# Kernel tuning notes

Hardware: AMD Instinct MI355X
Metric: run time of the kernel (lower is better)

Reference implementation:

```python
import jax, jax.numpy as jnp
import numpy as np

N = 100_000      # nodes
E = 1_600_000    # edges (avg degree 16)
H = 128          # hidden_dim
L = 2            # num_layers
G = 64           # graphs in batch
BN_EPS = 1e-5


def setup_inputs() -> dict:
    key = jax.random.key(0)
    ks = jax.random.split(key, 20)
    x = jax.random.normal(ks[0], (N, 1), jnp.float32)
    edge_index = jax.random.randint(ks[1], (2, E), 0, N, dtype=jnp.int64)
    edge_attr = jax.random.uniform(ks[2], (E, 1), jnp.float32)
    batch = jnp.sort(jax.random.randint(ks[3], (N,), 0, G, dtype=jnp.int64))
    s = 1.0 / np.sqrt(H)
    return {
        "x": x, "edge_index": edge_index, "edge_attr": edge_attr, "batch": batch,
        "enc_w": jax.random.normal(ks[4], (1, H), jnp.float32),
        "enc_b": jnp.zeros((H,), jnp.float32),
        "eenc_w": jax.random.normal(ks[5], (1, H), jnp.float32),
        "eenc_b": jnp.zeros((H,), jnp.float32),
        "eps": jnp.zeros((L,), jnp.float32),  # train_eps=True, init 0
        "w1": jax.random.normal(ks[6], (L, H, H), jnp.float32) * s,
        "b1": jnp.zeros((L, H), jnp.float32),
        "w2": jax.random.normal(ks[7], (L, H, H), jnp.float32) * s,
        "b2": jnp.zeros((L, H), jnp.float32),
        "gamma": jnp.ones((L, H), jnp.float32),
        "beta": jnp.zeros((L, H), jnp.float32),
        "cw1": jax.random.normal(ks[8], (H, H // 2), jnp.float32) * s,
        "cb1": jnp.zeros((H // 2,), jnp.float32),
        "cw2": jax.random.normal(ks[9], (H // 2, 1), jnp.float32) * (1.0 / np.sqrt(H // 2)),
        "cb2": jnp.zeros((1,), jnp.float32),
    }


def reference(x, edge_index, edge_attr, batch,
              enc_w, enc_b, eenc_w, eenc_b,
              eps, w1, b1, w2, b2, gamma, beta,
              cw1, cb1, cw2, cb2):
    # Inference mode: dropout = identity, BatchNorm uses running stats (mean=0, var=1).
    h = x @ enc_w + enc_b                 # [N, H] node encoder
    ea = edge_attr @ eenc_w + eenc_b      # [E, H] edge encoder
    src, dst = edge_index[0], edge_index[1]
    inv_std = 1.0 / jnp.sqrt(1.0 + BN_EPS)
    for l in range(L):
        # GINEConv: out = MLP((1+eps)*x + sum_j relu(x_j + e_ij))
        msg = jax.nn.relu(h[src] + ea)                         # [E, H] gather + fuse
        agg = jax.ops.segment_sum(msg, dst, num_segments=N)    # [N, H] scatter-sum
        z = (1.0 + eps[l]) * h + agg
        z = jax.nn.relu(z @ w1[l] + b1[l]) @ w2[l] + b2[l]      # GIN MLP
        h = jax.nn.relu(gamma[l] * z * inv_std + beta[l])       # BN (eval) + ReLU
    # global mean pool over graphs
    cnt = jax.ops.segment_sum(jnp.ones((N, 1), h.dtype), batch, num_segments=G)
    pooled = jax.ops.segment_sum(h, batch, num_segments=G) / jnp.maximum(cnt, 1.0)
    hc = jax.nn.relu(pooled @ cw1 + cb1)
    out = jax.nn.sigmoid(hc @ cw2 + cb2)
    return out.squeeze(-1)                # [G]
```

## Files before the change

### kernel.cpp

```cpp
#include <hip/hip_runtime.h>

#define HDIM 128
#define NGRAPH 64
#define INVSTD 0.99999500003749972f
#define WTPAD 136
#define WSLOT (128 * WTPAD)
#define BKN 512
#define EPB 4096

typedef unsigned short ushort_t;
typedef unsigned int uint_t;
typedef unsigned char uchar_t;
typedef __attribute__((ext_vector_type(8))) short bf16x8;
typedef __attribute__((ext_vector_type(4))) float f32x4;
typedef __attribute__((ext_vector_type(2))) float f32x2;

__device__ __forceinline__ float bf2f(uint_t u) {
    return __int_as_float((int)(u << 16));
}
__device__ __forceinline__ float bf2f_hi(uint_t u) {
    return __int_as_float((int)(u & 0xFFFF0000u));
}
__device__ __forceinline__ uint_t f2bf(float f) {
    uint_t x = __float_as_uint(f);
    return (x + 0x7FFFu + ((x >> 16) & 1u)) >> 16;
}
__device__ __forceinline__ uint_t pack2(float a, float b) {
    return f2bf(a) | (f2bf(b) << 16);
}
__device__ __forceinline__ uint_t pack4fp8(float a, float b, float c, float d) {
    int v = __builtin_amdgcn_cvt_pk_fp8_f32(a, b, 0, false);
    v = __builtin_amdgcn_cvt_pk_fp8_f32(c, d, v, true);
    return (uint_t)v;
}

__global__ void k_encode(const float* __restrict__ x, const float* __restrict__ ew,
                         const float* __restrict__ enb, const float* __restrict__ ebe,
                         ushort_t* __restrict__ hb, uchar_t* __restrict__ hq, int N) {
    int tid = blockIdx.x * blockDim.x + threadIdx.x;
    int stride = gridDim.x * blockDim.x;
    int q = tid & 15;
    float4 wa = ((const float4*)ew)[2 * q];
    float4 wb = ((const float4*)ew)[2 * q + 1];
    float4 ba = ((const float4*)enb)[2 * q];
    float4 bb = ((const float4*)enb)[2 * q + 1];
    float4 ea = ((const float4*)ebe)[2 * q];
    float4 eb2 = ((const float4*)ebe)[2 * q + 1];
    ba.x += ea.x; ba.y += ea.y; ba.z += ea.z; ba.w += ea.w;
    bb.x += eb2.x; bb.y += eb2.y; bb.z += eb2.z; bb.w += eb2.w;
    int total = N * 16;
    for (int t = tid; t < total; t += stride) {
        int n = t >> 4;
        float xv = x[n];
        float v0 = fmaf(xv, wa.x, ba.x), v1 = fmaf(xv, wa.y, ba.y);
        float v2 = fmaf(xv, wa.z, ba.z), v3 = fmaf(xv, wa.w, ba.w);
        float v4 = fmaf(xv, wb.x, bb.x), v5 = fmaf(xv, wb.y, bb.y);
        float v6 = fmaf(xv, wb.z, bb.z), v7 = fmaf(xv, wb.w, bb.w);
        uint4 o;
        o.x = pack2(v0, v1); o.y = pack2(v2, v3);
        o.z = pack2(v4, v5); o.w = pack2(v6, v7);
        ((uint4*)(hb + (size_t)n * HDIM))[q] = o;
        uint2 o8;
        o8.x = pack4fp8(v0, v1, v2, v3);
        o8.y = pack4fp8(v4, v5, v6, v7);
        ((uint2*)(hq + (size_t)n * HDIM))[q] = o8;
    }
}

__global__ void k_prepw(const float* __restrict__ w1, const float* __restrict__ w2,
                        ushort_t* __restrict__ wtg) {
    int t = blockIdx.x * 256 + threadIdx.x;
    if (t >= 4 * 16384) return;
    int w = t >> 14, idx = t & 16383;
    int k = idx >> 7, n = idx & 127;
    const float* src = ((w & 1) ? w2 : w1) + (size_t)(w >> 1) * 16384;
    wtg[(size_t)w * WSLOT + n * WTPAD + k] = (ushort_t)f2bf(src[idx]);
}

__global__ __launch_bounds__(256) void k_cnt(const int* __restrict__ ei, int* __restrict__ btot,
                                             int nb, int E) {
    __shared__ int hist[256];
    hist[threadIdx.x] = 0;
    __syncthreads();
    int e0 = blockIdx.x * EPB;
    for (int i = threadIdx.x; i < EPB; i += 256) {
        int e = e0 + i;
        if (e < E) atomicAdd(&hist[ei[E + e] / BKN], 1);
    }
    __syncthreads();
    int c = hist[threadIdx.x];
    if (threadIdx.x < nb && c > 0) atomicAdd(&btot[threadIdx.x], c);
}

__global__ void k_bscan(const int* __restrict__ btot, int* __restrict__ segs, int nb, int E) {
    __shared__ int sm[256];
    int t = threadIdx.x;
    int v = (t < nb) ? btot[t] : 0;
    sm[t] = v;
    __syncthreads();
    #pragma unroll
    for (int off = 1; off < 256; off <<= 1) {
        int u = (t >= off) ? sm[t - off] : 0;
        __syncthreads();
        sm[t] += u;
        __syncthreads();
    }
    if (t < nb) segs[t] = sm[t] - v;
    if (t == 0) segs[nb] = E;
}

__global__ __launch_bounds__(256) void k_place0(const int* __restrict__ ei,
                                                const float* __restrict__ attr,
                                                const int* __restrict__ segs, int* cursor,
                                                int4* __restrict__ ebuf, int nb, int E) {
    __shared__ int hist[256];
    __shared__ int basev[256];
    hist[threadIdx.x] = 0;
    __syncthreads();
    int e0 = blockIdx.x * EPB;
    for (int i = threadIdx.x; i < EPB; i += 256) {
        int e = e0 + i;
        if (e < E) atomicAdd(&hist[ei[E + e] / BKN], 1);
    }
    __syncthreads();
    {
        int c = hist[threadIdx.x];
        basev[threadIdx.x] = (threadIdx.x < nb && c > 0) ? atomicAdd(&cursor[threadIdx.x], c) : 0;
        hist[threadIdx.x] = 0;
    }
    __syncthreads();
    for (int i = threadIdx.x; i < EPB; i += 256) {
        int e = e0 + i;
        if (e < E) {
            int s = ei[e], d = ei[E + e];
            float a = attr[e];
            int b = d / BKN;
            int r = atomicAdd(&hist[b], 1);
            ebuf[segs[b] + basev[b] + r] = make_int4(s, __float_as_int(a), d, 0);
        }
    }
}

__global__ __launch_bounds__(256) void k_fine(const int4* __restrict__ ebuf,
                                              const int* __restrict__ segs,
                                              int2* __restrict__ epack, int* __restrict__ rs,
                                              int nb, int N, int E) {
    __shared__ int hist[BKN];
    __shared__ int cur[BKN];
    __shared__ int psum[256];
    int b = blockIdx.x;
    int d0 = b * BKN;
    int nd = min(BKN, N - d0);
    for (int i = threadIdx.x; i < BKN; i += 256) hist[i] = 0;
    __syncthreads();
    int s0 = segs[b], s1 = segs[b + 1];
    for (int e = s0 + threadIdx.x; e < s1; e += 256)
        atomicAdd(&hist[ebuf[e].z - d0], 1);
    __syncthreads();
    int h0 = hist[2 * threadIdx.x], h1 = hist[2 * threadIdx.x + 1];
    psum[threadIdx.x] = h0 + h1;
    __syncthreads();
    #pragma unroll
    for (int off = 1; off < 256; off <<= 1) {
        int u = (threadIdx.x >= off) ? psum[threadIdx.x - off] : 0;
        __syncthreads();
        psum[threadIdx.x] += u;
        __syncthreads();
    }
    int pb = psum[threadIdx.x] - (h0 + h1);
    cur[2 * threadIdx.x] = pb;
    cur[2 * threadIdx.x + 1] = pb + h0;
    __syncthreads();
    for (int i = threadIdx.x; i < nd; i += 256) rs[d0 + i] = s0 + cur[i];
    if (b == nb - 1 && threadIdx.x == 0) rs[N] = E;
    __syncthreads();
    for (int e = s0 + threadIdx.x; e < s1; e += 256) {
        int4 rec = ebuf[e];
        int r = atomicAdd(&cur[rec.z - d0], 1);
        epack[s0 + r] = make_int2(rec.x, rec.y);
    }
}

__device__ __forceinline__ void acc_edge(float acc[8], const uint2& u, float at,
        const float4& wa, const float4& wb) {
    f32x2 p0 = __builtin_amdgcn_cvt_pk_f32_fp8(u.x, false);
    f32x2 p1 = __builtin_amdgcn_cvt_pk_f32_fp8(u.x, true);
    f32x2 p2 = __builtin_amdgcn_cvt_pk_f32_fp8(u.y, false);
    f32x2 p3 = __builtin_amdgcn_cvt_pk_f32_fp8(u.y, true);
    acc[0] += fmaxf(fmaf(at, wa.x, p0[0]), 0.f);
    acc[1] += fmaxf(fmaf(at, wa.y, p0[1]), 0.f);
    acc[2] += fmaxf(fmaf(at, wa.z, p1[0]), 0.f);
    acc[3] += fmaxf(fmaf(at, wa.w, p1[1]), 0.f);
    acc[4] += fmaxf(fmaf(at, wb.x, p2[0]), 0.f);
    acc[5] += fmaxf(fmaf(at, wb.y, p2[1]), 0.f);
    acc[6] += fmaxf(fmaf(at, wb.z, p3[0]), 0.f);
    acc[7] += fmaxf(fmaf(at, wb.w, p3[1]), 0.f);
}

__global__ __launch_bounds__(256) void k_agg(
    const uchar_t* __restrict__ hq, const ushort_t* __restrict__ hb,
    const int* __restrict__ rs, const int2* __restrict__ epack,
    const float* __restrict__ ew, const float* __restrict__ ebv,
    const float* __restrict__ epsp, ushort_t* __restrict__ zb, int N) {
    int wave = (blockIdx.x * 256 + threadIdx.x) >> 6;
    if (wave >= N) return;
    int lane = threadIdx.x & 63;
    int p = lane >> 4;
    int q = lane & 15;
    int n = wave;
    int beg = rs[n];
    int cntE = rs[n + 1] - beg;
    float4 wa = ((const float4*)ew)[2 * q], wb = ((const float4*)ew)[2 * q + 1];

    float acc[8] = {0.f, 0.f, 0.f, 0.f, 0.f, 0.f, 0.f, 0.f};
    float acc2[8] = {0.f, 0.f, 0.f, 0.f, 0.f, 0.f, 0.f, 0.f};
    int j = p;
    for (; j + 4 < cntE; j += 8) {
        int2 e1 = epack[beg + j];
        int2 e2 = epack[beg + j + 4];
        uint2 u1 = *(const uint2*)(hq + (size_t)e1.x * HDIM + q * 8);
        uint2 u2 = *(const uint2*)(hq + (size_t)e2.x * HDIM + q * 8);
        acc_edge(acc,  u1, __int_as_float(e1.y), wa, wb);
        acc_edge(acc2, u2, __int_as_float(e2.y), wa, wb);
    }
    if (j < cntE) {
        int2 e1 = epack[beg + j];
        uint2 u1 = *(const uint2*)(hq + (size_t)e1.x * HDIM + q * 8);
        acc_edge(acc, u1, __int_as_float(e1.y), wa, wb);
    }
    #pragma unroll
    for (int k = 0; k < 8; ++k) {
        float v = acc[k] + acc2[k];
        v += __shfl_xor(v, 16);
        v += __shfl_xor(v, 32);
        acc[k] = v;
    }
    if (p == 0) {
        float sc = 1.f + epsp[0];
        float4 ba = ((const float4*)ebv)[2 * q], bb = ((const float4*)ebv)[2 * q + 1];
        float s0 = sc * ba.x, s1 = sc * ba.y, s2 = sc * ba.z, s3 = sc * ba.w;
        float s4 = sc * bb.x, s5 = sc * bb.y, s6 = sc * bb.z, s7 = sc * bb.w;
        uint4 u = *(const uint4*)(hb + (size_t)n * HDIM + q * 8);
        uint4 ob;
        ob.x = pack2(fmaf(sc, bf2f(u.x & 0xFFFFu), acc[0]) - s0,
                     fmaf(sc, bf2f_hi(u.x),        acc[1]) - s1);
        ob.y = pack2(fmaf(sc, bf2f(u.y & 0xFFFFu), acc[2]) - s2,
                     fmaf(sc, bf2f_hi(u.y),        acc[3]) - s3);
        ob.z = pack2(fmaf(sc, bf2f(u.z & 0xFFFFu), acc[4]) - s4,
                     fmaf(sc, bf2f_hi(u.z),        acc[5]) - s5);
        ob.w = pack2(fmaf(sc, bf2f(u.w & 0xFFFFu), acc[6]) - s6,
                     fmaf(sc, bf2f_hi(u.w),        acc[7]) - s7);
        *(uint4*)(zb + (size_t)n * HDIM + q * 8) = ob;
    }
}

template<int MODE, int EBF, int WQ>
__global__ __launch_bounds__(256) void k_gemm(
    const ushort_t* __restrict__ A, const ushort_t* __restrict__ WT,
    const float* __restrict__ bias, const float* __restrict__ gam,
    const float* __restrict__ bet, const float* __restrict__ ebe,
    ushort_t* __restrict__ out, uchar_t* __restrict__ outq, int N) {
    __shared__ ushort_t wt[128 * WTPAD];
    int tid = threadIdx.x;
    #pragma unroll
    for (int i = 0; i < 9; ++i) {
        int c = i * 256 + tid;
        if (c < 2176) ((bf16x8*)wt)[c] = ((const bf16x8*)WT)[c];
    }
    __syncthreads();

    int wid = tid >> 6, lane = tid & 63;
    int ra = lane & 15, qa = lane >> 4;

    bf16x8 bfr[4][8];
    #pragma unroll
    for (int ks = 0; ks < 4; ++ks)
        #pragma unroll
        for (int nf = 0; nf < 8; ++nf)
            bfr[ks][nf] = *(const bf16x8*)&wt[(nf * 16 + ra) * WTPAD + ks * 32 + qa * 8];

    float bi[8], gg[8], be_[8], ef[8];
    #pragma unroll
    for (int nf = 0; nf < 8; ++nf) {
        int col = nf * 16 + ra;
        bi[nf] = bias[col];
        if (MODE == 1) { gg[nf] = gam[col]; be_[nf] = bet[col]; }
        if (EBF)       { ef[nf] = ebe[col]; }
    }

    bf16x8 azero;
    #pragma unroll
    for (int j = 0; j < 8; ++j) azero[j] = 0;

    #pragma unroll
    for (int it = 0; it < 4; ++it) {
        int m0 = blockIdx.x * 256 + it * 64 + wid * 16;
        int mr = m0 + ra;
        bf16x8 afr[4];
        #pragma unroll
        for (int ks = 0; ks < 4; ++ks)
            afr[ks] = (mr < N) ? *(const bf16x8*)&A[(size_t)mr * HDIM + ks * 32 + qa * 8]
                               : azero;
        f32x4 acc[8];
        #pragma unroll
        for (int nf = 0; nf < 8; ++nf)
            #pragma unroll
            for (int j = 0; j < 4; ++j) acc[nf][j] = 0.f;
        #pragma unroll
        for (int ks = 0; ks < 4; ++ks)
            #pragma unroll
            for (int nf = 0; nf < 8; ++nf)
                acc[nf] = __builtin_amdgcn_mfma_f32_16x16x32_bf16(afr[ks], bfr[ks][nf], acc[nf], 0, 0, 0);
        #pragma unroll
        for (int nf = 0; nf < 8; ++nf) {
            #pragma unroll
            for (int r = 0; r < 4; ++r) {
                int row = m0 + qa * 4 + r;
                if (row < N) {
                    float v = acc[nf][r] + bi[nf];
                    if (MODE == 0) v = fmaxf(v, 0.f);
                    else           v = fmaxf(fmaf(gg[nf] * v, INVSTD, be_[nf]), 0.f);
                    if (EBF)       v += ef[nf];
                    out[(size_t)row * HDIM + nf * 16 + ra] = (ushort_t)f2bf(v);
                    if (WQ)
                        outq[(size_t)row * HDIM + nf * 16 + ra] =
                            (uchar_t)(__builtin_amdgcn_cvt_pk_fp8_f32(v, 0.f, 0, false) & 0xFF);
                }
            }
        }
    }
}

#define PCHUNK 256
#define PWIN 4
__global__ __launch_bounds__(256) void k_pool2(const ushort_t* __restrict__ hb,
                                               const int* __restrict__ batch,
                                               float* pooled, int N) {
    __shared__ float acc[PWIN][HDIM];
    int n0 = blockIdx.x * PCHUNK;
    if (n0 >= N) return;
    int n1 = min(n0 + PCHUNK, N);
    int g0 = batch[n0];
    int g1 = batch[n1 - 1];
    for (int i = threadIdx.x; i < PWIN * HDIM; i += 256) ((float*)acc)[i] = 0.f;
    __syncthreads();

    int grp = threadIdx.x >> 5;
    int q = threadIdx.x & 31;
    float4 racc = make_float4(0.f, 0.f, 0.f, 0.f);
    int gcur = g0;
    for (int n = n0 + grp; n < n1; n += 8) {
        int g = batch[n];
        if (g != gcur) {
            int w = gcur - g0;
            float* p = (w < PWIN) ? &acc[w][q * 4] : (pooled + gcur * HDIM + q * 4);
            atomicAdd(p + 0, racc.x); atomicAdd(p + 1, racc.y);
            atomicAdd(p + 2, racc.z); atomicAdd(p + 3, racc.w);
            racc = make_float4(0.f, 0.f, 0.f, 0.f);
            gcur = g;
        }
        uint2 u = ((const uint2*)(hb + (size_t)n * HDIM))[q];
        racc.x += bf2f(u.x);
        racc.y += bf2f_hi(u.x);
        racc.z += bf2f(u.y);
        racc.w += bf2f_hi(u.y);
    }
    {
        int w = gcur - g0;
        float* p = (w < PWIN) ? &acc[w][q * 4] : (pooled + gcur * HDIM + q * 4);
        atomicAdd(p + 0, racc.x); atomicAdd(p + 1, racc.y);
        atomicAdd(p + 2, racc.z); atomicAdd(p + 3, racc.w);
    }
    __syncthreads();

    int span = min(g1 - g0 + 1, PWIN);
    for (int i = threadIdx.x; i < span * HDIM; i += 256) {
        int w = i >> 7, f = i & 127;
        float v = acc[w][f];
        if (v != 0.f) atomicAdd(pooled + (g0 + w) * HDIM + f, v);
    }
}

__global__ void k_classify(const float* __restrict__ pooled, const int* __restrict__ batch,
                           const float* __restrict__ cw1, const float* __restrict__ cb1,
                           const float* __restrict__ cw2, const float* __restrict__ cb2,
                           float* __restrict__ out, int N) {
    __shared__ float p[HDIM];
    int g = blockIdx.x, j = threadIdx.x;
    int lo = 0, hi = N;
    while (lo < hi) { int m = (lo + hi) >> 1; if (batch[m] < g) lo = m + 1; else hi = m; }
    int lo2 = lo, hi2 = N;
    while (lo2 < hi2) { int m = (lo2 + hi2) >> 1; if (batch[m] < g + 1) lo2 = m + 1; else hi2 = m; }
    float c = fmaxf((float)(lo2 - lo), 1.f);
    p[j]      = pooled[g * HDIM + j] / c;
    p[j + 64] = pooled[g * HDIM + j + 64] / c;
    __syncthreads();
    float acc = cb1[j];
    #pragma unroll 4
    for (int k = 0; k < HDIM; ++k) acc = fmaf(p[k], cw1[k * 64 + j], acc);
    acc = fmaxf(acc, 0.f);
    float v = acc * cw2[j];
    #pragma unroll
    for (int off = 32; off > 0; off >>= 1) v += __shfl_down(v, off, 64);
    if (j == 0) out[g] = 1.f / (1.f + expf(-(v + cb2[0])));
}

static inline size_t align_up(size_t v, size_t a) { return (v + a - 1) & ~(a - 1); }

extern "C" void kernel_launch(void* const* d_in, const int* in_sizes, int n_in,
                              void* d_out, int out_size, void* d_ws, size_t ws_size,
                              hipStream_t stream) {
    const float* x      = (const float*)d_in[0];
    const int*   ei     = (const int*)d_in[1];
    const float* eattr  = (const float*)d_in[2];
    const int*   batch  = (const int*)d_in[3];
    const float* enc_w  = (const float*)d_in[4];
    const float* enc_b  = (const float*)d_in[5];
    const float* eenc_w = (const float*)d_in[6];
    const float* eenc_b = (const float*)d_in[7];
    const float* eps    = (const float*)d_in[8];
    const float* w1     = (const float*)d_in[9];
    const float* b1     = (const float*)d_in[10];
    const float* w2     = (const float*)d_in[11];
    const float* b2     = (const float*)d_in[12];
    const float* gamma  = (const float*)d_in[13];
    const float* beta   = (const float*)d_in[14];
    const float* cw1    = (const float*)d_in[15];
    const float* cb1    = (const float*)d_in[16];
    const float* cw2    = (const float*)d_in[17];
    const float* cb2    = (const float*)d_in[18];

    int N = in_sizes[0];
    int E = in_sizes[2];

    int nb = (N + BKN - 1) / BKN;
    int nblk = (E + EPB - 1) / EPB;

    char* wsb = (char*)d_ws;
    size_t off = 0;
    ushort_t* hb  = (ushort_t*)(wsb + off); off = align_up(off + (size_t)N * HDIM * 2, 256);
    uchar_t*  hq  = (uchar_t*)(wsb + off);  off = align_up(off + (size_t)N * HDIM, 256);
    ushort_t* zb  = (ushort_t*)(wsb + off); off = align_up(off + (size_t)N * HDIM * 2, 256);
    ushort_t* wtg = (ushort_t*)(wsb + off); off = align_up(off + (size_t)4 * WSLOT * 2, 256);
    float* pooled = (float*)(wsb + off);    off = align_up(off + NGRAPH * HDIM * 4, 256);
    int*   btot   = (int*)(wsb + off);      off = align_up(off + (size_t)(nb + 1) * 4, 256);
    int*   segs   = (int*)(wsb + off);      off = align_up(off + (size_t)(nb + 1) * 4, 256);
    int*   cursor = (int*)(wsb + off);      off = align_up(off + (size_t)nb * 4, 256);
    int*   rs     = (int*)(wsb + off);      off = align_up(off + (size_t)(N + 1) * 4, 256);
    int4*  ebuf   = (int4*)(wsb + off);     off = align_up(off + (size_t)E * 16, 256);
    int2*  epack  = (int2*)(wsb + off);     off = align_up(off + (size_t)E * 8, 256);

    hipMemsetAsync(btot, 0, (size_t)(nb + 1) * 4, stream);
    hipMemsetAsync(cursor, 0, (size_t)nb * 4, stream);
    k_cnt<<<nblk, 256, 0, stream>>>(ei, btot, nb, E);
    k_prepw<<<256, 256, 0, stream>>>(w1, w2, wtg);
    k_bscan<<<1, 256, 0, stream>>>(btot, segs, nb, E);
    k_place0<<<nblk, 256, 0, stream>>>(ei, eattr, segs, cursor, ebuf, nb, E);
    k_fine<<<nb, 256, 0, stream>>>(ebuf, segs, epack, rs, nb, N, E);

    hipMemsetAsync(pooled, 0, NGRAPH * HDIM * sizeof(float), stream);
    k_encode<<<2048, 256, 0, stream>>>(x, enc_w, enc_b, eenc_b, hb, hq, N);

    int gblocks = (N + 255) / 256;
    int ablocks = (N * 64 + 255) / 256;

    k_agg<<<ablocks, 256, 0, stream>>>(hq, hb, rs, epack, eenc_w, eenc_b, eps + 0, zb, N);
    k_gemm<0,0,0><<<gblocks, 256, 0, stream>>>(zb, wtg + 0 * WSLOT, b1, nullptr, nullptr,
                                               nullptr, zb, nullptr, N);
    k_gemm<1,1,1><<<gblocks, 256, 0, stream>>>(zb, wtg + 1 * WSLOT, b2, gamma, beta,
                                               eenc_b, hb, hq, N);
    k_agg<<<ablocks, 256, 0, stream>>>(hq, hb, rs, epack, eenc_w, eenc_b, eps + 1, zb, N);
    k_gemm<0,0,0><<<gblocks, 256, 0, stream>>>(zb, wtg + 2 * WSLOT, b1 + HDIM, nullptr, nullptr,
                                               nullptr, zb, nullptr, N);
    k_gemm<1,0,0><<<gblocks, 256, 0, stream>>>(zb, wtg + 3 * WSLOT, b2 + HDIM, gamma + HDIM,
                                               beta + HDIM, nullptr, hb, nullptr, N);

    k_pool2<<<(N + PCHUNK - 1) / PCHUNK, 256, 0, stream>>>(hb, batch, pooled, N);
    k_classify<<<NGRAPH, 64, 0, stream>>>(pooled, batch, cw1, cb1, cw2, cb2, (float*)d_out, N);
}
```

Before: 302.9 us.

## Fuse the two GIN MLP GEMMs into one kernel with intermediate in LDS

Merges the two per-layer GEMM launches into a single k_mlp kernel. Each wave computes its 16-row tile of the first linear+ReLU and writes it to its own slice of shared memory, then runs the second GEMM with the BN, ReLU and output epilogue from there. This removes a global round trip of the intermediate activation and one launch per layer. In exchange, weight fragments are now read directly from global memory per wave instead of being staged in LDS, and each block covers fewer rows.

```diff
diff --git a/kernel.cpp b/kernel.cpp
--- a/kernel.cpp
+++ b/kernel.cpp
@@ -254,47 +254,32 @@
     }
 }
 
-template<int MODE, int EBF, int WQ>
-__global__ __launch_bounds__(256) void k_gemm(
-    const ushort_t* __restrict__ A, const ushort_t* __restrict__ WT,
-    const float* __restrict__ bias, const float* __restrict__ gam,
-    const float* __restrict__ bet, const float* __restrict__ ebe,
+template<int EBF, int WQ>
+__global__ __launch_bounds__(512) void k_mlp(
+    const ushort_t* __restrict__ A, const ushort_t* __restrict__ WT1,
+    const ushort_t* __restrict__ WT2,
+    const float* __restrict__ b1v, const float* __restrict__ b2v,
+    const float* __restrict__ gam, const float* __restrict__ bet,
+    const float* __restrict__ ebe,
     ushort_t* __restrict__ out, uchar_t* __restrict__ outq, int N) {
-    __shared__ ushort_t wt[128 * WTPAD];
+    __shared__ ushort_t tls[128 * WTPAD];
     int tid = threadIdx.x;
-    #pragma unroll
-    for (int i = 0; i < 9; ++i) {
-        int c = i * 256 + tid;
-        if (c < 2176) ((bf16x8*)wt)[c] = ((const bf16x8*)WT)[c];
-    }
-    __syncthreads();
-
     int wid = tid >> 6, lane = tid & 63;
     int ra = lane & 15, qa = lane >> 4;
-
-    bf16x8 bfr[4][8];
-    #pragma unroll
-    for (int ks = 0; ks < 4; ++ks)
-        #pragma unroll
-        for (int nf = 0; nf < 8; ++nf)
-            bfr[ks][nf] = *(const bf16x8*)&wt[(nf * 16 + ra) * WTPAD + ks * 32 + qa * 8];
-
-    float bi[8], gg[8], be_[8], ef[8];
-    #pragma unroll
-    for (int nf = 0; nf < 8; ++nf) {
-        int col = nf * 16 + ra;
-        bi[nf] = bias[col];
-        if (MODE == 1) { gg[nf] = gam[col]; be_[nf] = bet[col]; }
-        if (EBF)       { ef[nf] = ebe[col]; }
-    }
+    int m0 = blockIdx.x * 128 + wid * 16;
+    ushort_t* tw = &tls[wid * 16 * WTPAD];
 
     bf16x8 azero;
     #pragma unroll
     for (int j = 0; j < 8; ++j) azero[j] = 0;
 
-    #pragma unroll
-    for (int it = 0; it < 4; ++it) {
-        int m0 = blockIdx.x * 256 + it * 64 + wid * 16;
+    {
+        bf16x8 bfr[4][8];
+        #pragma unroll
+        for (int ks = 0; ks < 4; ++ks)
+            #pragma unroll
+            for (int nf = 0; nf < 8; ++nf)
+                bfr[ks][nf] = *(const bf16x8*)&WT1[(nf * 16 + ra) * WTPAD + ks * 32 + qa * 8];
         int mr = m0 + ra;
         bf16x8 afr[4];
         #pragma unroll
@@ -313,17 +298,52 @@
                 acc[nf] = __builtin_amdgcn_mfma_f32_16x16x32_bf16(afr[ks], bfr[ks][nf], acc[nf], 0, 0, 0);
         #pragma unroll
         for (int nf = 0; nf < 8; ++nf) {
+            float bi = b1v[nf * 16 + ra];
+            #pragma unroll
+            for (int r = 0; r < 4; ++r) {
+                int lr = qa * 4 + r;
+                float v = fmaxf(acc[nf][r] + bi, 0.f);
+                tw[lr * WTPAD + nf * 16 + ra] = (ushort_t)f2bf(v);
+            }
+        }
+    }
+
+    {
+        bf16x8 bfr[4][8];
+        #pragma unroll
+        for (int ks = 0; ks < 4; ++ks)
+            #pragma unroll
+            for (int nf = 0; nf < 8; ++nf)
+                bfr[ks][nf] = *(const bf16x8*)&WT2[(nf * 16 + ra) * WTPAD + ks * 32 + qa * 8];
+        bf16x8 afr[4];
+        #pragma unroll
+        for (int ks = 0; ks < 4; ++ks)
+            afr[ks] = *(const bf16x8*)&tw[ra * WTPAD + ks * 32 + qa * 8];
+        f32x4 acc[8];
+        #pragma unroll
+        for (int nf = 0; nf < 8; ++nf)
+            #pragma unroll
+            for (int j = 0; j < 4; ++j) acc[nf][j] = 0.f;
+        #pragma unroll
+        for (int ks = 0; ks < 4; ++ks)
+            #pragma unroll
+            for (int nf = 0; nf < 8; ++nf)
+                acc[nf] = __builtin_amdgcn_mfma_f32_16x16x32_bf16(afr[ks], bfr[ks][nf], acc[nf], 0, 0, 0);
+        #pragma unroll
+        for (int nf = 0; nf < 8; ++nf) {
+            int col = nf * 16 + ra;
+            float bi = b2v[col];
+            float gg = gam[col], be_ = bet[col];
+            float ef = EBF ? ebe[col] : 0.f;
             #pragma unroll
             for (int r = 0; r < 4; ++r) {
                 int row = m0 + qa * 4 + r;
                 if (row < N) {
-                    float v = acc[nf][r] + bi[nf];
-                    if (MODE == 0) v = fmaxf(v, 0.f);
-                    else           v = fmaxf(fmaf(gg[nf] * v, INVSTD, be_[nf]), 0.f);
-                    if (EBF)       v += ef[nf];
-                    out[(size_t)row * HDIM + nf * 16 + ra] = (ushort_t)f2bf(v);
+                    float v = fmaxf(fmaf(gg * (acc[nf][r] + bi), INVSTD, be_), 0.f);
+                    if (EBF) v += ef;
+                    out[(size_t)row * HDIM + col] = (ushort_t)f2bf(v);
                     if (WQ)
-                        outq[(size_t)row * HDIM + nf * 16 + ra] =
+                        outq[(size_t)row * HDIM + col] =
                             (uchar_t)(__builtin_amdgcn_cvt_pk_fp8_f32(v, 0.f, 0, false) & 0xFF);
                 }
             }
@@ -461,19 +481,16 @@
     hipMemsetAsync(pooled, 0, NGRAPH * HDIM * sizeof(float), stream);
     k_encode<<<2048, 256, 0, stream>>>(x, enc_w, enc_b, eenc_b, hb, hq, N);
 
-    int gblocks = (N + 255) / 256;
+    int mblocks = (N + 127) / 128;
     int ablocks = (N * 64 + 255) / 256;
 
     k_agg<<<ablocks, 256, 0, stream>>>(hq, hb, rs, epack, eenc_w, eenc_b, eps + 0, zb, N);
-    k_gemm<0,0,0><<<gblocks, 256, 0, stream>>>(zb, wtg + 0 * WSLOT, b1, nullptr, nullptr,
-                                               nullptr, zb, nullptr, N);
-    k_gemm<1,1,1><<<gblocks, 256, 0, stream>>>(zb, wtg + 1 * WSLOT, b2, gamma, beta,
-                                               eenc_b, hb, hq, N);
+    k_mlp<1,1><<<mblocks, 512, 0, stream>>>(zb, wtg + 0 * WSLOT, wtg + 1 * WSLOT,
+                                            b1, b2, gamma, beta, eenc_b, hb, hq, N);
     k_agg<<<ablocks, 256, 0, stream>>>(hq, hb, rs, epack, eenc_w, eenc_b, eps + 1, zb, N);
-    k_gemm<0,0,0><<<gblocks, 256, 0, stream>>>(zb, wtg + 2 * WSLOT, b1 + HDIM, nullptr, nullptr,
-                                               nullptr, zb, nullptr, N);
-    k_gemm<1,0,0><<<gblocks, 256, 0, stream>>>(zb, wtg + 3 * WSLOT, b2 + HDIM, gamma + HDIM,
-                                               beta + HDIM, nullptr, hb, nullptr, N);
+    k_mlp<0,0><<<mblocks, 512, 0, stream>>>(zb, wtg + 2 * WSLOT, wtg + 3 * WSLOT,
+                                            b1 + HDIM, b2 + HDIM, gamma + HDIM, beta + HDIM,
+                                            nullptr, hb, nullptr, N);
 
     k_pool2<<<(N + PCHUNK - 1) / PCHUNK, 256, 0, stream>>>(hb, batch, pooled, N);
     k_classify<<<NGRAPH, 64, 0, stream>>>(pooled, batch, cw1, cb1, cw2, cb2, (float*)d_out, N);
```

After: 345.5 us. 1.14x slower.
